# Kernel tuning notes

Measured on AMD Instinct MI355X. Metric: run time of the kernel, lower is better.

Reference implementation:

```python
import jax, jax.numpy as jnp
import numpy as np

B, T, N, FIN, FOUT, EDGE_DIM = 8, 16, 256, 32, 32, 16


def setup_inputs() -> dict:
    key = jax.random.key(0)
    ks = jax.random.split(key, 8)
    def xavier(k, shape):
        fan_in, fan_out = shape[0], shape[1]
        limit = float(np.sqrt(6.0 / (fan_in + fan_out)))
        return jax.random.uniform(k, shape, jnp.float32, -limit, limit)
    return {
        "x": jax.random.normal(ks[0], (B, T, N, FIN), jnp.float32),
        "adj": jax.random.uniform(ks[1], (N, N), jnp.float32),
        # edge_net: Linear(1, edge_dim) -> GELU -> Linear(edge_dim, Fin*Fout)
        "w1": xavier(ks[2], (1, EDGE_DIM)),
        "b1": jnp.zeros((EDGE_DIM,), jnp.float32),
        "w2": xavier(ks[3], (EDGE_DIM, FIN * FOUT)),
        "b2": jnp.zeros((FIN * FOUT,), jnp.float32),
        # node_lin: Linear(Fin, Fout)
        "node_w": xavier(ks[4], (FIN, FOUT)),
        "node_b": jnp.zeros((FOUT,), jnp.float32),
    }


def reference(x, adj, w1, b1, w2, b2, node_w, node_b):
    # edge-conditioned weights: (N, N, Fin, Fout)
    h = jax.nn.gelu(adj[:, :, None] * w1[0] + b1, approximate=False)  # (N,N,E)
    edge_w = (h @ w2 + b2).reshape(N, N, FIN, FOUT)
    # msg[b,t,i,j,:] = sum_f x[b,t,j,f] * edge_w[i,j,f,:]; agg = sum_j msg
    agg = jnp.einsum("btjf,ijfo->btio", x, edge_w)  # (B,T,N,Fout)
    y = jax.nn.gelu(x @ node_w + node_b + agg, approximate=False)
    return y
```

## Files before the change

### kernel.cpp

```cpp
#include <hip/hip_runtime.h>
#include <math.h>

#define NB    256
#define FINN  32
#define FOUTN 32
#define BT    128


typedef __attribute__((ext_vector_type(8))) short short8;
typedef __attribute__((ext_vector_type(4))) float floatx4;

#define MFMA16(a,b,c) __builtin_amdgcn_mfma_f32_16x16x32_bf16((a),(b),(c),0,0,0)

#define BARRIER() asm volatile("s_waitcnt lgkmcnt(0)\n\ts_barrier" ::: "memory")

__device__ __forceinline__ float gelu_f(float v) {
    return 0.5f * v * (1.0f + erff(v * 0.70710678118654752f));
}
__device__ __forceinline__ ushort f2bf(float x) {
    union { float f; unsigned u; } v; v.f = x;
    unsigned r = (v.u + 0x7FFFu + ((v.u >> 16) & 1u)) >> 16;
    return (ushort)r;
}
__device__ __forceinline__ float bf2f(ushort b) {
    union { unsigned u; float f; } v; v.u = ((unsigned)b) << 16; return v.f;
}
__device__ __forceinline__ uint2 pack4(floatx4 d) {
    uint2 p;
    p.x = (unsigned)f2bf(d[0]) | ((unsigned)f2bf(d[1]) << 16);
    p.y = (unsigned)f2bf(d[2]) | ((unsigned)f2bf(d[3]) << 16);
    return p;
}

__global__ __launch_bounds__(256) void prep_kernel(
        const float* __restrict__ x,   const float* __restrict__ adj,
        const float* __restrict__ w1,  const float* __restrict__ b1,
        const float* __restrict__ w2,  const float* __restrict__ b2,
        const float* __restrict__ node_w, const float* __restrict__ node_b,
        ushort* __restrict__ Hf, ushort* __restrict__ w2f,
        ushort* __restrict__ xaf, ushort* __restrict__ nwf,
        float* __restrict__ bias2g) {
    int bid = blockIdx.x;
    int tid = threadIdx.x;

    if (bid < 128) {
        __shared__ float adjs[16][264];
        __shared__ float w1s[16], b1s[16];
        int it = bid & 15;
        int kq8 = bid >> 4;
        if (tid < 16) { w1s[tid] = w1[tid]; b1s[tid] = b1[tid]; }
        #pragma unroll
        for (int q = 0; q < 4; ++q) {
            int u = q * 256 + tid;
            int row = u >> 6, c4 = u & 63;
            *(float4*)&adjs[row][c4 * 4] =
                ((const float4*)(adj + ((size_t)it * 16 + row) * 256))[c4];
        }
        __syncthreads();
        #pragma unroll
        for (int q = 0; q < 4; ++q) {
            int u = q * 256 + tid;
            int ks = kq8 * 16 + (u >> 6);
            int lane = u & 63;
            int m = lane & 15, quad = lane >> 4;
            int e = ks >> 3;
            int j0 = (ks & 7) * 32 + quad * 8;
            float w = w1s[e], b = b1s[e];
            ushort tmp[8];
            #pragma unroll
            for (int d = 0; d < 8; ++d)
                tmp[d] = f2bf(gelu_f(adjs[m][j0 + d] * w + b));
            *(int4*)(Hf + (((size_t)it * 128 + ks) * 64 + lane) * 8) = *(int4*)tmp;
        }
        return;
    }
    if (bid < 160) {
        int wv = tid >> 6, lane = tid & 63, m = lane & 15, quad = lane >> 4;
        int bt = (bid - 128) * 4 + wv;
        #pragma unroll
        for (int jt = 0; jt < 16; ++jt) {
            const float* xs = x + ((size_t)bt * NB + jt * 16 + m) * FINN + quad * 8;
            float4 lo = *(const float4*)xs;
            float4 hi = *(const float4*)(xs + 4);
            ushort tmp[8];
            tmp[0]=f2bf(lo.x); tmp[1]=f2bf(lo.y); tmp[2]=f2bf(lo.z); tmp[3]=f2bf(lo.w);
            tmp[4]=f2bf(hi.x); tmp[5]=f2bf(hi.y); tmp[6]=f2bf(hi.z); tmp[7]=f2bf(hi.w);
            *(int4*)(xaf + (((size_t)bt * 16 + jt) * 64 + lane) * 8) = *(int4*)tmp;
        }
        return;
    }
    if (bid < 288) {
        __shared__ float Sp[8][32];
        __shared__ float Svs[32];
        int bt = bid - 160;
        int f = tid & 31, grp = tid >> 5;
        float s = 0.f;
        for (int j = grp; j < NB; j += 8)
            s += x[((size_t)bt * NB + j) * FINN + f];
        Sp[grp][f] = s;
        __syncthreads();
        if (tid < 32) {
            float s2 = 0.f;
            #pragma unroll
            for (int g = 0; g < 8; ++g) s2 += Sp[g][tid];
            Svs[tid] = s2;
        }
        __syncthreads();
        if (tid < 32) {
            float bb = node_b[tid];
            #pragma unroll
            for (int f2 = 0; f2 < FINN; ++f2)
                bb += Svs[f2] * b2[f2 * FOUTN + tid];
            bias2g[bt * 32 + tid] = bb;
        }
        return;
    }
    for (int s = 0; s < 2048; s += 256) {
        int slot = s + tid;
        int e = slot >> 7, r = slot & 127;
        int ot = r >> 6, lane = r & 63;
        int m = lane & 15, quad = lane >> 4;
        const float* src = w2 + (size_t)e * 1024 + (quad * 8) * 32 + ot * 16 + m;
        ushort tmp[8];
        #pragma unroll
        for (int i = 0; i < 8; ++i) tmp[i] = f2bf(src[i * 32]);
        *(int4*)(w2f + (size_t)slot * 8) = *(int4*)tmp;
    }
    if (tid < 128) {
        int ot = tid >> 6, lane = tid & 63, m = lane & 15, q = lane >> 4;
        ushort tmp[8];
        #pragma unroll
        for (int d = 0; d < 8; ++d)
            tmp[d] = f2bf(node_w[(q * 8 + d) * 32 + ot * 16 + m]);
        *(int4*)(nwf + tid * 8) = *(int4*)tmp;
    }
}

__global__ __launch_bounds__(512, 4) void main_kernel(
        const ushort* __restrict__ Hf,  const ushort* __restrict__ w2f,
        const ushort* __restrict__ xaf, float* __restrict__ Cp) {
    __shared__ ushort Bsl[2][8][2][512];

    int bt   = blockIdx.x;
    int kq   = blockIdx.y;
    int tid  = threadIdx.x;
    int wv   = tid >> 6;
    int lane = tid & 63;
    int m    = lane & 15;
    int quad = lane >> 4;

    short8 xfr[2];
    #pragma unroll
    for (int t = 0; t < 2; ++t)
        xfr[t] = *(const short8*)(xaf + (((size_t)bt * 16 + wv + 8 * t) * 64 + lane) * 8);
    short8 wfr[4][2];
    #pragma unroll
    for (int e_ = 0; e_ < 4; ++e_)
        #pragma unroll
        for (int ot = 0; ot < 2; ++ot)
            wfr[e_][ot] = *(const short8*)(w2f + (size_t)(kq * 4 + e_) * 1024
                                           + ot * 512 + lane * 8);

    short8 areg[2][2];
    floatx4 acc[2][2] = {};

    #define ALOADS(pp, s_)                                                    \
    {                                                                         \
        int ks_ = kq * 32 + (s_);                                             \
        areg[pp][0] = *(const short8*)(Hf + (((size_t)(2 * wv + 0) * 128 + ks_) * 64 + lane) * 8); \
        areg[pp][1] = *(const short8*)(Hf + (((size_t)(2 * wv + 1) * 128 + ks_) * 64 + lane) * 8); \
    }
    #define PRODUCE(buf, w_)                                                  \
    {                                                                         \
        int qc = (wv & 1) * 2 + (quad >> 1);                                  \
        int dp = (quad & 1) * 4;                                              \
        _Pragma("unroll")                                                     \
        for (int t = 0; t < 2; ++t) {                                         \
            int jp = (wv >> 1) + 4 * t;                                       \
            floatx4 z = {0.f, 0.f, 0.f, 0.f};                                 \
            floatx4 d0 = MFMA16(xfr[t], wfr[w_][0], z);                       \
            floatx4 d1 = MFMA16(xfr[t], wfr[w_][1], z);                       \
            *(uint2*)&Bsl[buf][jp][0][(qc * 16 + m) * 8 + dp] = pack4(d0);    \
            *(uint2*)&Bsl[buf][jp][1][(qc * 16 + m) * 8 + dp] = pack4(d1);    \
        }                                                                     \
    }
    #define GEMMC(buf, w_)                                                    \
    {                                                                         \
        _Pragma("unroll")                                                     \
        for (int kk = 0; kk < 8; ++kk) {                                      \
            int s = (w_) * 8 + kk;                                            \
            if (s < 31) ALOADS((s + 1) & 1, s + 1);                           \
            short8 b0 = *(const short8*)&Bsl[buf][kk][0][lane * 8];           \
            short8 b1 = *(const short8*)&Bsl[buf][kk][1][lane * 8];           \
            acc[0][0] = MFMA16(areg[s & 1][0], b0, acc[0][0]);                \
            acc[0][1] = MFMA16(areg[s & 1][0], b1, acc[0][1]);                \
            acc[1][0] = MFMA16(areg[s & 1][1], b0, acc[1][0]);                \
            acc[1][1] = MFMA16(areg[s & 1][1], b1, acc[1][1]);                \
        }                                                                     \
    }

    ALOADS(0, 0);
    PRODUCE(0, 0);
    BARRIER();
    #pragma unroll
    for (int w = 0; w < 4; ++w) {
        if (w < 3) PRODUCE((w + 1) & 1, w + 1);
        GEMMC(w & 1, w);
        BARRIER();
    }

    #pragma unroll
    for (int t = 0; t < 2; ++t)
        #pragma unroll
        for (int oh = 0; oh < 2; ++oh)
            #pragma unroll
            for (int r = 0; r < 4; ++r) {
                int i = (2 * wv + t) * 16 + quad * 4 + r;
                Cp[(((size_t)kq * BT + bt) * NB + i) * FOUTN + oh * 16 + m]
                    = acc[t][oh][r];
            }
    #undef ALOADS
    #undef PRODUCE
    #undef GEMMC
}

__global__ __launch_bounds__(256) void epi_kernel(
        const ushort* __restrict__ xaf, const ushort* __restrict__ nwf,
        const float* __restrict__ bias2g, const float* __restrict__ Cp,
        float* __restrict__ out) {
    int bt   = blockIdx.x;
    int tid  = threadIdx.x;
    int wv   = tid >> 6;
    int lane = tid & 63;
    int m    = lane & 15;
    int quad = lane >> 4;

    short8 nb0 = *(const short8*)(nwf + (size_t)lane * 8);
    short8 nb1 = *(const short8*)(nwf + ((size_t)64 + lane) * 8);

    #pragma unroll
    for (int t = 0; t < 4; ++t) {
        int it = wv * 4 + t;
        short8 xa = *(const short8*)(xaf + (((size_t)bt * 16 + it) * 64 + lane) * 8);
        #pragma unroll
        for (int tn = 0; tn < 2; ++tn) {
            floatx4 z = {0.f, 0.f, 0.f, 0.f};
            floatx4 ea = MFMA16(xa, tn ? nb1 : nb0, z);
            float bz = bias2g[bt * 32 + tn * 16 + m];
            #pragma unroll
            for (int r = 0; r < 4; ++r) {
                int i = it * 16 + quad * 4 + r;
                float s = ea[r] + bz;
                #pragma unroll
                for (int kqi = 0; kqi < 4; ++kqi)
                    s += Cp[(((size_t)kqi * BT + bt) * NB + i) * FOUTN + tn * 16 + m];
                out[((size_t)bt * NB + i) * FOUTN + tn * 16 + m] = gelu_f(s);
            }
        }
    }
}

extern "C" void kernel_launch(void* const* d_in, const int* in_sizes, int n_in,
                              void* d_out, int out_size, void* d_ws, size_t ws_size,
                              hipStream_t stream) {
    const float* x      = (const float*)d_in[0];
    const float* adj    = (const float*)d_in[1];
    const float* w1     = (const float*)d_in[2];
    const float* b1     = (const float*)d_in[3];
    const float* w2     = (const float*)d_in[4];
    const float* b2     = (const float*)d_in[5];
    const float* node_w = (const float*)d_in[6];
    const float* node_b = (const float*)d_in[7];
    float* out = (float*)d_out;

    ushort* Hf     = (ushort*)d_ws;
    ushort* w2f    = Hf + (size_t)16 * 128 * 512;
    ushort* xaf    = w2f + 16384;
    ushort* nwf    = xaf + (size_t)128 * 16 * 512;
    float*  bias2g = (float*)(nwf + 1024);
    float*  Cp     = bias2g + 128 * 32;

    hipLaunchKernelGGL(prep_kernel, dim3(289), dim3(256), 0, stream,
                       x, adj, w1, b1, w2, b2, node_w, node_b,
                       Hf, w2f, xaf, nwf, bias2g);
    hipLaunchKernelGGL(main_kernel, dim3(BT, 4), dim3(512), 0, stream,
                       Hf, w2f, xaf, Cp);
    hipLaunchKernelGGL(epi_kernel, dim3(BT), dim3(256), 0, stream,
                       xaf, nwf, bias2g, Cp, out);
}
```

Measured before the change: 109.9 us.

## Restructure main kernel pipeline with deeper A prefetch and split epilogue grid

The main loop is no longer fully unrolled. A-fragment prefetch goes from double to 4-deep register buffering, and w2 fragments are loaded per stage instead of all held upfront, which cuts register pressure. The production of the next B tile now runs after the current GEMM instead of before it. The partial-sum layout Cp is changed so the four kq partials sit next to each other for the epilogue. The epilogue grid is doubled to 2 blocks per bt for more parallelism. The risk is less overlap from the rolled loop, plus extra clamped loads past the end.

```diff
diff --git a/kernel.cpp b/kernel.cpp
--- a/kernel.cpp
+++ b/kernel.cpp
@@ -21,9 +21,6 @@
     union { float f; unsigned u; } v; v.f = x;
     unsigned r = (v.u + 0x7FFFu + ((v.u >> 16) & 1u)) >> 16;
     return (ushort)r;
-}
-__device__ __forceinline__ float bf2f(ushort b) {
-    union { unsigned u; float f; } v; v.u = ((unsigned)b) << 16; return v.f;
 }
 __device__ __forceinline__ uint2 pack4(floatx4 d) {
     uint2 p;
@@ -153,59 +150,66 @@
     #pragma unroll
     for (int t = 0; t < 2; ++t)
         xfr[t] = *(const short8*)(xaf + (((size_t)bt * 16 + wv + 8 * t) * 64 + lane) * 8);
-    short8 wfr[4][2];
-    #pragma unroll
-    for (int e_ = 0; e_ < 4; ++e_)
-        #pragma unroll
-        for (int ot = 0; ot < 2; ++ot)
-            wfr[e_][ot] = *(const short8*)(w2f + (size_t)(kq * 4 + e_) * 1024
-                                           + ot * 512 + lane * 8);
-
-    short8 areg[2][2];
+    const int qc = (wv & 1) * 2 + (quad >> 1);
+    const int dp = (quad & 1) * 4;
+    const int jp0 = (wv >> 1);
+
+    const ushort* Ha = Hf + ((size_t)(2 * wv + 0) * 128) * 512 + (size_t)lane * 8;
+    const ushort* Hb = Hf + ((size_t)(2 * wv + 1) * 128) * 512 + (size_t)lane * 8;
+    const ushort* Wl = w2f + (size_t)lane * 8;
+
+    short8 areg[4][2];
     floatx4 acc[2][2] = {};
 
-    #define ALOADS(pp, s_)                                                    \
+    #define ALOADS(slot, s_)                                                  \
     {                                                                         \
-        int ks_ = kq * 32 + (s_);                                             \
-        areg[pp][0] = *(const short8*)(Hf + (((size_t)(2 * wv + 0) * 128 + ks_) * 64 + lane) * 8); \
-        areg[pp][1] = *(const short8*)(Hf + (((size_t)(2 * wv + 1) * 128 + ks_) * 64 + lane) * 8); \
-    }
-    #define PRODUCE(buf, w_)                                                  \
+        int ks_ = kq * 32 + (s_); if (ks_ > 127) ks_ = 127;                   \
+        areg[slot][0] = *(const short8*)(Ha + (size_t)ks_ * 512);             \
+        areg[slot][1] = *(const short8*)(Hb + (size_t)ks_ * 512);             \
+    }
+    #define PRODUCE(bp, wf0, wf1)                                             \
     {                                                                         \
-        int qc = (wv & 1) * 2 + (quad >> 1);                                  \
-        int dp = (quad & 1) * 4;                                              \
         _Pragma("unroll")                                                     \
         for (int t = 0; t < 2; ++t) {                                         \
-            int jp = (wv >> 1) + 4 * t;                                       \
+            int jp = jp0 + 4 * t;                                             \
             floatx4 z = {0.f, 0.f, 0.f, 0.f};                                 \
-            floatx4 d0 = MFMA16(xfr[t], wfr[w_][0], z);                       \
-            floatx4 d1 = MFMA16(xfr[t], wfr[w_][1], z);                       \
-            *(uint2*)&Bsl[buf][jp][0][(qc * 16 + m) * 8 + dp] = pack4(d0);    \
-            *(uint2*)&Bsl[buf][jp][1][(qc * 16 + m) * 8 + dp] = pack4(d1);    \
+            floatx4 d0 = MFMA16(xfr[t], wf0, z);                              \
+            floatx4 d1 = MFMA16(xfr[t], wf1, z);                              \
+            *(uint2*)((bp) + jp * 1024 +       (qc * 16 + m) * 8 + dp) = pack4(d0); \
+            *(uint2*)((bp) + jp * 1024 + 512 + (qc * 16 + m) * 8 + dp) = pack4(d1); \
         }                                                                     \
     }
-    #define GEMMC(buf, w_)                                                    \
-    {                                                                         \
-        _Pragma("unroll")                                                     \
-        for (int kk = 0; kk < 8; ++kk) {                                      \
-            int s = (w_) * 8 + kk;                                            \
-            if (s < 31) ALOADS((s + 1) & 1, s + 1);                           \
-            short8 b0 = *(const short8*)&Bsl[buf][kk][0][lane * 8];           \
-            short8 b1 = *(const short8*)&Bsl[buf][kk][1][lane * 8];           \
-            acc[0][0] = MFMA16(areg[s & 1][0], b0, acc[0][0]);                \
-            acc[0][1] = MFMA16(areg[s & 1][0], b1, acc[0][1]);                \
-            acc[1][0] = MFMA16(areg[s & 1][1], b0, acc[1][0]);                \
-            acc[1][1] = MFMA16(areg[s & 1][1], b1, acc[1][1]);                \
-        }                                                                     \
-    }
 
     ALOADS(0, 0);
-    PRODUCE(0, 0);
+    ALOADS(1, 1);
+    {
+        short8 wf0 = *(const short8*)(Wl + (size_t)(kq * 4) * 1024);
+        short8 wf1 = *(const short8*)(Wl + (size_t)(kq * 4) * 1024 + 512);
+        PRODUCE((ushort*)Bsl, wf0, wf1);
+    }
     BARRIER();
-    #pragma unroll
+
+    #pragma unroll 1
     for (int w = 0; w < 4; ++w) {
-        if (w < 3) PRODUCE((w + 1) & 1, w + 1);
-        GEMMC(w & 1, w);
+        int en = kq * 4 + ((w < 3) ? (w + 1) : 3);
+        short8 wf0 = *(const short8*)(Wl + (size_t)en * 1024);
+        short8 wf1 = *(const short8*)(Wl + (size_t)en * 1024 + 512);
+
+        ushort* Bb = (ushort*)Bsl + (w & 1) * 8192;
+        #pragma unroll
+        for (int kk = 0; kk < 8; ++kk) {
+            ALOADS((kk + 2) & 3, w * 8 + kk + 2);
+            short8 b0 = *(const short8*)(Bb + kk * 1024 + lane * 8);
+            short8 b1 = *(const short8*)(Bb + kk * 1024 + 512 + lane * 8);
+            acc[0][0] = MFMA16(areg[kk & 3][0], b0, acc[0][0]);
+            acc[0][1] = MFMA16(areg[kk & 3][0], b1, acc[0][1]);
+            acc[1][0] = MFMA16(areg[kk & 3][1], b0, acc[1][0]);
+            acc[1][1] = MFMA16(areg[kk & 3][1], b1, acc[1][1]);
+        }
+        if (w < 3) {
+            ushort* Bn = (ushort*)Bsl + ((w + 1) & 1) * 8192;
+            PRODUCE(Bn, wf0, wf1);
+        }
         BARRIER();
     }
 
@@ -216,12 +220,11 @@
             #pragma unroll
             for (int r = 0; r < 4; ++r) {
                 int i = (2 * wv + t) * 16 + quad * 4 + r;
-                Cp[(((size_t)kq * BT + bt) * NB + i) * FOUTN + oh * 16 + m]
+                Cp[(((size_t)bt * NB + i) * 4 + kq) * FOUTN + oh * 16 + m]
                     = acc[t][oh][r];
             }
     #undef ALOADS
     #undef PRODUCE
-    #undef GEMMC
 }
 
 __global__ __launch_bounds__(256) void epi_kernel(
@@ -229,6 +232,7 @@
         const float* __restrict__ bias2g, const float* __restrict__ Cp,
         float* __restrict__ out) {
     int bt   = blockIdx.x;
+    int ih   = blockIdx.y;
     int tid  = threadIdx.x;
     int wv   = tid >> 6;
     int lane = tid & 63;
@@ -239,8 +243,8 @@
     short8 nb1 = *(const short8*)(nwf + ((size_t)64 + lane) * 8);
 
     #pragma unroll
-    for (int t = 0; t < 4; ++t) {
-        int it = wv * 4 + t;
+    for (int t = 0; t < 2; ++t) {
+        int it = ih * 8 + wv * 2 + t;
         short8 xa = *(const short8*)(xaf + (((size_t)bt * 16 + it) * 64 + lane) * 8);
         #pragma unroll
         for (int tn = 0; tn < 2; ++tn) {
@@ -253,7 +257,7 @@
                 float s = ea[r] + bz;
                 #pragma unroll
                 for (int kqi = 0; kqi < 4; ++kqi)
-                    s += Cp[(((size_t)kqi * BT + bt) * NB + i) * FOUTN + tn * 16 + m];
+                    s += Cp[(((size_t)bt * NB + i) * 4 + kqi) * FOUTN + tn * 16 + m];
                 out[((size_t)bt * NB + i) * FOUTN + tn * 16 + m] = gelu_f(s);
             }
         }
@@ -285,6 +289,6 @@
                        Hf, w2f, xaf, nwf, bias2g);
     hipLaunchKernelGGL(main_kernel, dim3(BT, 4), dim3(512), 0, stream,
                        Hf, w2f, xaf, Cp);
-    hipLaunchKernelGGL(epi_kernel, dim3(BT), dim3(256), 0, stream,
+    hipLaunchKernelGGL(epi_kernel, dim3(BT, 2), dim3(256), 0, stream,
                        xaf, nwf, bias2g, Cp, out);
 }
```

New measurement: 104.6 us. 4.9% less time.
